# Kernel tuning notes

Hardware: AMD Instinct MI355X
Metric: run time of the kernel (lower is better)

The kernel has to match this reference:

```python
import jax, jax.numpy as jnp
import numpy as np

WINDOW = 10
STRIDES = 1
EPS = 1e-5


def setup_inputs() -> dict:
    key = jax.random.key(0)
    B, T, F = 128, 512, 40
    tensors = jax.random.normal(key, (B, T, F), dtype=jnp.float32)
    return {"tensors": tensors}


def reference(tensors):
    # tensors: [B, T, F]
    B, T, F = tensors.shape
    # window start positions, replicating the module's iter_list logic
    starts = np.arange(0, T - WINDOW + 1, STRIDES)
    if (T - WINDOW) not in starts:
        starts = np.append(starts, T - WINDOW)
    # [S, W] gather indices -> windowed view [B, S, W, F]
    idx = starts[:, None] + np.arange(WINDOW)[None, :]
    xw = tensors[:, idx, :]  # [B, S, W, F]

    mean = xw.mean(axis=2)  # [B, S, F] == K.mean over window axis
    # K.std: population std (ddof=0) over the window axis
    std = jnp.sqrt(((xw - mean[:, :, None, :]) ** 2).mean(axis=2))  # [B, S, F]
    # K.switch(is_nan(std), mean-mean, std): NaN std -> 0
    std = jnp.where(jnp.isnan(std), jnp.zeros_like(std), std) + EPS

    # E[x_i * x_j] over window for all feature pairs: [B, S, F, F]
    Exy = jnp.einsum('bswi,bswj->bsij', xw, xw) / WINDOW
    cov = Exy - mean[:, :, :, None] * mean[:, :, None, :]
    corr = cov / (std[:, :, :, None] * std[:, :, None, :])  # [B, S, F, F]

    # itertools.combinations(range(F), 2) order == upper-triangular row-major
    iu, ju = np.triu_indices(F, 1)
    return corr[:, :, iu, ju]  # [B, S, C] with C = F*(F-1)/2
```

## Files before the change

kernel.cpp:

```cpp
#include <hip/hip_runtime.h>
#include <hip/hip_fp16.h>

#define BB   128
#define TT   512
#define FF   40
#define WW   10
#define NS   503
#define NP   780
#define SC   64
#define NCHUNK 8
#define ROWS (SC + WW - 1)
#define NT   512
#define EPSC 1e-5f
#define C01  0.31622776601683794f

__global__ __launch_bounds__(NT, 8) void ts_corr_r13(const float* __restrict__ in,
                                                     float* __restrict__ out) {
    const int blk = blockIdx.x;
    const int b   = blk >> 3;
    const int c   = blk & (NCHUNK - 1);
    const int s0  = (c == NCHUNK - 1) ? (NS - SC) : c * SC;
    const int tid = threadIdx.x;

    __shared__ float   xs[SC + WW][FF];
    __shared__ __half2 st[SC][FF];

    const float4* src4 = (const float4*)(in + ((size_t)b * TT + s0) * FF);
    float4* xs4 = (float4*)&xs[0][0];
    {
        xs4[tid] = src4[tid];
        const int i2 = tid + NT;
        if (i2 < ROWS * FF / 4) xs4[i2] = src4[i2];
    }
    __syncthreads();

    #pragma unroll
    for (int k = 0; k < 2; ++k) {
        const int qd = tid + k * NT;
        if (qd < SC * FF / 4) {
            const int t  = qd / 10;
            const int f0 = (qd - t * 10) * 4;
            float sx0=0,sx1=0,sx2=0,sx3=0, sq0=0,sq1=0,sq2=0,sq3=0;
            #pragma unroll
            for (int w = 0; w < WW; ++w) {
                const float4 x = *(const float4*)&xs[t + w][f0];
                sx0 += x.x; sx1 += x.y; sx2 += x.z; sx3 += x.w;
                sq0 += x.x*x.x; sq1 += x.y*x.y; sq2 += x.z*x.z; sq3 += x.w*x.w;
            }
            const float m0 = sx0*0.1f, m1 = sx1*0.1f, m2 = sx2*0.1f, m3 = sx3*0.1f;
            const float u0 = 1.f/(sqrtf(fmaxf(sq0*0.1f - m0*m0, 0.f)) + EPSC);
            const float u1 = 1.f/(sqrtf(fmaxf(sq1*0.1f - m1*m1, 0.f)) + EPSC);
            const float u2 = 1.f/(sqrtf(fmaxf(sq2*0.1f - m2*m2, 0.f)) + EPSC);
            const float u3 = 1.f/(sqrtf(fmaxf(sq3*0.1f - m3*m3, 0.f)) + EPSC);
            st[t][f0]     = __floats2half2_rn(u0*C01, m0*u0);
            st[t][f0 + 1] = __floats2half2_rn(u1*C01, m1*u1);
            st[t][f0 + 2] = __floats2half2_rn(u2*C01, m2*u2);
            st[t][f0 + 3] = __floats2half2_rn(u3*C01, m3*u3);
        }
    }

    int pi[2], pj[2];
    float sxy[2], ph[2][WW];
    #pragma unroll
    for (int k = 0; k < 2; ++k) {
        const int p = tid + k * NT;
        const int pp = (p < NP) ? p : 0;
        int i = (int)((79.0f - sqrtf((float)(6241 - 8 * pp))) * 0.5f);
        while (i > 0 && i * (79 - i) / 2 > pp) --i;
        while ((i + 1) * (79 - (i + 1)) / 2 <= pp) ++i;
        pi[k] = i;
        pj[k] = pp - i * (79 - i) / 2 + i + 1;
        float s = 0.f;
        #pragma unroll
        for (int w = 0; w < WW; ++w) {
            const float pr = xs[w][pi[k]] * xs[w][pj[k]];
            ph[k][w] = pr;
            s += pr;
        }
        sxy[k] = s;
    }
    __syncthreads();

    const bool act1 = (tid < NP - NT);
    float* dst0 = out + (size_t)(b * NS + s0) * NP + tid;

#define SLOT(K, OFF) do {                                                       \
    const int _ii = pi[K], _jj = pj[K];                                         \
    const float  _xiA = xs[_tA + WW][_ii], _xiB = xs[_tA + WW + 1][_ii];        \
    const float  _xjA = xs[_tA + WW][_jj], _xjB = xs[_tA + WW + 1][_jj];        \
    const float2 _siA = __half22float2(st[_tA][_ii]);                           \
    const float2 _siB = __half22float2(st[_tA + 1][_ii]);                       \
    const float2 _sjA = __half22float2(st[_tA][_jj]);                           \
    const float2 _sjB = __half22float2(st[_tA + 1][_jj]);                       \
    _dA[OFF] = sxy[K] * _siA.x * _sjA.x - _siA.y * _sjA.y;                      \
    const float _pn = _xiA * _xjA;                                              \
    sxy[K] += _pn - ph[K][U]; ph[K][U] = _pn;                                   \
    _dB[OFF] = sxy[K] * _siB.x * _sjB.x - _siB.y * _sjB.y;                      \
    if (DO2) {                                                                  \
        const float _p2 = _xiB * _xjB;                                          \
        sxy[K] += _p2 - ph[K][(U) + 1]; ph[K][(U) + 1] = _p2;                   \
    }                                                                           \
} while (0)

#define STEP2(UU, TA, DD) do {                                                  \
    const int _tA = (TA);                                                       \
    const int U = (UU);                                                         \
    const bool DO2 = (DD);                                                      \
    float* _dA = dst0 + (size_t)_tA * NP;                                       \
    float* _dB = _dA + NP;                                                      \
    SLOT(0, 0);                                                                 \
    if (act1) SLOT(1, NT);                                                      \
} while (0)

    for (int t0 = 0; t0 < 60; t0 += WW) {
        STEP2(0, t0,     true);
        STEP2(2, t0 + 2, true);
        STEP2(4, t0 + 4, true);
        STEP2(6, t0 + 6, true);
        STEP2(8, t0 + 8, true);
    }
    STEP2(0, 60, true);
    STEP2(2, 62, false);
#undef STEP2
#undef SLOT
}

extern "C" void kernel_launch(void* const* d_in, const int* in_sizes, int n_in,
                              void* d_out, int out_size, void* d_ws, size_t ws_size,
                              hipStream_t stream) {
    const float* in = (const float*)d_in[0];
    float* out = (float*)d_out;
    ts_corr_r13<<<BB * NCHUNK, NT, 0, stream>>>(in, out);
}
```

Baseline: 44.06 us.

## Assign four consecutive pairs per thread and store results as float4

The block shrinks from 512 to 256 threads. Each of 195 active threads now owns four consecutive feature pairs (780 = 4*195) instead of up to two strided pairs, and writes each output row with 128-bit float4 stores. The aim is to cut store instruction count, avoid the idle half-warp second slot, and raise per-thread ILP. In exchange, 61 threads idle during the main loop, register use per thread rises with four running sums and product histories, and LDS reads become less regular across lanes.

```diff
diff --git a/kernel.cpp b/kernel.cpp
--- a/kernel.cpp
+++ b/kernel.cpp
@@ -10,12 +10,13 @@
 #define SC   64
 #define NCHUNK 8
 #define ROWS (SC + WW - 1)
-#define NT   512
+#define NT   256
+#define NQ   195
 #define EPSC 1e-5f
 #define C01  0.31622776601683794f
 
-__global__ __launch_bounds__(NT, 8) void ts_corr_r13(const float* __restrict__ in,
-                                                     float* __restrict__ out) {
+__global__ __launch_bounds__(NT) void ts_corr_r16(const float* __restrict__ in,
+                                                  float* __restrict__ out) {
     const int blk = blockIdx.x;
     const int b   = blk >> 3;
     const int c   = blk & (NCHUNK - 1);
@@ -27,15 +28,15 @@
 
     const float4* src4 = (const float4*)(in + ((size_t)b * TT + s0) * FF);
     float4* xs4 = (float4*)&xs[0][0];
-    {
-        xs4[tid] = src4[tid];
-        const int i2 = tid + NT;
-        if (i2 < ROWS * FF / 4) xs4[i2] = src4[i2];
+    #pragma unroll
+    for (int k = 0; k < 3; ++k) {
+        const int i = tid + k * NT;
+        if (i < ROWS * FF / 4) xs4[i] = src4[i];
     }
     __syncthreads();
 
     #pragma unroll
-    for (int k = 0; k < 2; ++k) {
+    for (int k = 0; k < 3; ++k) {
         const int qd = tid + k * NT;
         if (qd < SC * FF / 4) {
             const int t  = qd / 10;
@@ -59,57 +60,54 @@
         }
     }
 
-    int pi[2], pj[2];
-    float sxy[2], ph[2][WW];
+    int pi[4], pj[4];
+    float sxy[4], ph[4][WW];
+    const int pbase = 4 * min(tid, NQ - 1);
     #pragma unroll
-    for (int k = 0; k < 2; ++k) {
-        const int p = tid + k * NT;
-        const int pp = (p < NP) ? p : 0;
-        int i = (int)((79.0f - sqrtf((float)(6241 - 8 * pp))) * 0.5f);
-        while (i > 0 && i * (79 - i) / 2 > pp) --i;
-        while ((i + 1) * (79 - (i + 1)) / 2 <= pp) ++i;
-        pi[k] = i;
-        pj[k] = pp - i * (79 - i) / 2 + i + 1;
+    for (int q = 0; q < 4; ++q) {
+        const int p = pbase + q;
+        int i = (int)((79.0f - sqrtf((float)(6241 - 8 * p))) * 0.5f);
+        while (i > 0 && i * (79 - i) / 2 > p) --i;
+        while ((i + 1) * (79 - (i + 1)) / 2 <= p) ++i;
+        pi[q] = i;
+        pj[q] = p - i * (79 - i) / 2 + i + 1;
         float s = 0.f;
         #pragma unroll
         for (int w = 0; w < WW; ++w) {
-            const float pr = xs[w][pi[k]] * xs[w][pj[k]];
-            ph[k][w] = pr;
+            const float pr = xs[w][pi[q]] * xs[w][pj[q]];
+            ph[q][w] = pr;
             s += pr;
         }
-        sxy[k] = s;
+        sxy[q] = s;
     }
     __syncthreads();
 
-    const bool act1 = (tid < NP - NT);
-    float* dst0 = out + (size_t)(b * NS + s0) * NP + tid;
+    if (tid >= NQ) return;
 
-#define SLOT(K, OFF) do {                                                       \
-    const int _ii = pi[K], _jj = pj[K];                                         \
-    const float  _xiA = xs[_tA + WW][_ii], _xiB = xs[_tA + WW + 1][_ii];        \
-    const float  _xjA = xs[_tA + WW][_jj], _xjB = xs[_tA + WW + 1][_jj];        \
-    const float2 _siA = __half22float2(st[_tA][_ii]);                           \
-    const float2 _siB = __half22float2(st[_tA + 1][_ii]);                       \
-    const float2 _sjA = __half22float2(st[_tA][_jj]);                           \
-    const float2 _sjB = __half22float2(st[_tA + 1][_jj]);                       \
-    _dA[OFF] = sxy[K] * _siA.x * _sjA.x - _siA.y * _sjA.y;                      \
-    const float _pn = _xiA * _xjA;                                              \
-    sxy[K] += _pn - ph[K][U]; ph[K][U] = _pn;                                   \
-    _dB[OFF] = sxy[K] * _siB.x * _sjB.x - _siB.y * _sjB.y;                      \
-    if (DO2) {                                                                  \
-        const float _p2 = _xiB * _xjB;                                          \
-        sxy[K] += _p2 - ph[K][(U) + 1]; ph[K][(U) + 1] = _p2;                   \
+    float* dst0 = out + (size_t)(b * NS + s0) * NP + 4 * tid;
+
+#define STEP2(U, TA, DO2) do {                                                  \
+    float4 _vA, _vB;                                                            \
+    _Pragma("unroll")                                                           \
+    for (int q = 0; q < 4; ++q) {                                               \
+        const int _ii = pi[q], _jj = pj[q];                                     \
+        const float  _xiA = xs[(TA) + WW][_ii], _xiB = xs[(TA) + WW + 1][_ii];  \
+        const float  _xjA = xs[(TA) + WW][_jj], _xjB = xs[(TA) + WW + 1][_jj];  \
+        const float2 _siA = __half22float2(st[(TA)][_ii]);                      \
+        const float2 _siB = __half22float2(st[(TA) + 1][_ii]);                  \
+        const float2 _sjA = __half22float2(st[(TA)][_jj]);                      \
+        const float2 _sjB = __half22float2(st[(TA) + 1][_jj]);                  \
+        (&_vA.x)[q] = sxy[q] * _siA.x * _sjA.x - _siA.y * _sjA.y;               \
+        const float _pn = _xiA * _xjA;                                          \
+        sxy[q] += _pn - ph[q][U]; ph[q][U] = _pn;                               \
+        (&_vB.x)[q] = sxy[q] * _siB.x * _sjB.x - _siB.y * _sjB.y;               \
+        if (DO2) {                                                              \
+            const float _p2 = _xiB * _xjB;                                      \
+            sxy[q] += _p2 - ph[q][(U) + 1]; ph[q][(U) + 1] = _p2;               \
+        }                                                                       \
     }                                                                           \
-} while (0)
-
-#define STEP2(UU, TA, DD) do {                                                  \
-    const int _tA = (TA);                                                       \
-    const int U = (UU);                                                         \
-    const bool DO2 = (DD);                                                      \
-    float* _dA = dst0 + (size_t)_tA * NP;                                       \
-    float* _dB = _dA + NP;                                                      \
-    SLOT(0, 0);                                                                 \
-    if (act1) SLOT(1, NT);                                                      \
+    *(float4*)(dst0 + (size_t)(TA) * NP)     = _vA;                             \
+    *(float4*)(dst0 + (size_t)(TA + 1) * NP) = _vB;                             \
 } while (0)
 
     for (int t0 = 0; t0 < 60; t0 += WW) {
@@ -122,7 +120,6 @@
     STEP2(0, 60, true);
     STEP2(2, 62, false);
 #undef STEP2
-#undef SLOT
 }
 
 extern "C" void kernel_launch(void* const* d_in, const int* in_sizes, int n_in,
@@ -130,5 +127,5 @@
                               hipStream_t stream) {
     const float* in = (const float*)d_in[0];
     float* out = (float*)d_out;
-    ts_corr_r13<<<BB * NCHUNK, NT, 0, stream>>>(in, out);
+    ts_corr_r16<<<BB * NCHUNK, NT, 0, stream>>>(in, out);
 }
```

Result: slower. 47.83 us (+8.5%).
